# Performance work log

Measured on AMD Instinct MI355X. Metric: run time of the kernel, lower is better.

## Reference

```python
import jax, jax.numpy as jnp
import numpy as np

B, T, D, H, L, V = 2, 1024, 1024, 4, 4, 32000  # H redefined below
H = 16            # n_heads
HD = D // H       # head_size = 64
NL = 4            # n_layer
EPS = 1e-5


def _layernorm(x, scale, bias):
    mu = jnp.mean(x, axis=-1, keepdims=True)
    var = jnp.mean(jnp.square(x - mu), axis=-1, keepdims=True)
    return (x - mu) * jax.lax.rsqrt(var + EPS) * scale + bias


def setup_inputs() -> dict:
    key = jax.random.key(0)
    ks = iter(jax.random.split(key, 40))
    s = lambda shape: jax.random.normal(next(ks), shape, jnp.float32) * 0.02
    inp = {
        'idx': jax.random.randint(next(ks), (B, T), 0, V),
        'tok_emb': s((V, D)),
        'pos_emb': s((T, D)),
        # per-layer stacked params (leading axis = layer)
        'Wq': s((NL, D, D)), 'Wk': s((NL, D, D)), 'Wv': s((NL, D, D)),
        'Wo': s((NL, D, D)), 'bo': jnp.zeros((NL, D), jnp.float32),
        'ln1_s': jnp.ones((NL, D), jnp.float32), 'ln1_b': jnp.zeros((NL, D), jnp.float32),
        'ln2_s': jnp.ones((NL, D), jnp.float32), 'ln2_b': jnp.zeros((NL, D), jnp.float32),
        'W1': s((NL, D, 4 * D)), 'b1': jnp.zeros((NL, 4 * D), jnp.float32),
        'W2': s((NL, 4 * D, D)), 'b2': jnp.zeros((NL, D), jnp.float32),
        'lnf_s': jnp.ones((D,), jnp.float32), 'lnf_b': jnp.zeros((D,), jnp.float32),
        'Wlm': s((D, V)), 'blm': jnp.zeros((V,), jnp.float32),
    }
    return inp


def reference(idx, tok_emb, pos_emb, Wq, Wk, Wv, Wo, bo,
              ln1_s, ln1_b, ln2_s, ln2_b, W1, b1, W2, b2,
              lnf_s, lnf_b, Wlm, blm):
    b, t = idx.shape
    x = tok_emb[idx] + pos_emb[None, :t]            # [B,T,D]
    causal = jnp.tril(jnp.ones((t, t), bool))        # [T,T]
    scale = 1.0 / np.sqrt(HD).astype(np.float32)
    for l in range(NL):
        h = _layernorm(x, ln1_s[l], ln1_b[l])
        q = (h @ Wq[l]).reshape(b, t, H, HD)
        k = (h @ Wk[l]).reshape(b, t, H, HD)
        v = (h @ Wv[l]).reshape(b, t, H, HD)
        scores = jnp.einsum('bthd,bshd->bhts', q, k) * scale
        scores = jnp.where(causal[None, None], scores, -jnp.inf)
        attn = jax.nn.softmax(scores, axis=-1)       # [B,H,T,T]
        o = jnp.einsum('bhts,bshd->bthd', attn, v).reshape(b, t, D)
        x = x + o @ Wo[l] + bo[l]
        h2 = _layernorm(x, ln2_s[l], ln2_b[l])
        x = x + jax.nn.relu(h2 @ W1[l] + b1[l]) @ W2[l] + b2[l]
    x = _layernorm(x, lnf_s, lnf_b)
    logits = x @ Wlm + blm                           # [B,T,V]
    return logits
```

## Files before the change

### kernel.cpp

```cpp
#include <hip/hip_runtime.h>

typedef unsigned short u16;
typedef unsigned int u32;
typedef __bf16 bf16x8 __attribute__((ext_vector_type(8)));
typedef float f32x4 __attribute__((ext_vector_type(4)));
typedef u16 u16x8 __attribute__((ext_vector_type(8)));
typedef u16 u16x4 __attribute__((ext_vector_type(4)));

static __device__ __forceinline__ u16 f2bf(float f) {
  u32 u = __builtin_bit_cast(u32, f);
  u32 r = (u + 0x7FFFu + ((u >> 16) & 1u)) >> 16;
  return (u16)r;
}

static __device__ __forceinline__ void atomAddF32(float* p, float v) {
  asm volatile("global_atomic_add_f32 %0, %1, off" :: "v"(p), "v"(v) : "memory");
}

#define GLOAD_LDS16(gp, lp)                                                   \
  __builtin_amdgcn_global_load_lds(                                           \
      (const __attribute__((address_space(1))) void*)(gp),                    \
      (__attribute__((address_space(3))) void*)(lp), 16, 0, 0)

__global__ void k_embed_ln(const int* __restrict__ idx, const float* __restrict__ tok,
                           const float* __restrict__ pos, const float* __restrict__ sc,
                           const float* __restrict__ bi, float* __restrict__ x,
                           u16* __restrict__ out) {
  int row = blockIdx.x;
  int tt = row & 1023;
  int id = idx[row];
  int t = threadIdx.x;
  float4 a = *(const float4*)(tok + (size_t)id * 1024 + t * 4);
  float4 p = *(const float4*)(pos + (size_t)tt * 1024 + t * 4);
  float4 v{a.x + p.x, a.y + p.y, a.z + p.z, a.w + p.w};
  *(float4*)(x + (size_t)row * 1024 + t * 4) = v;
  float s = v.x + v.y + v.z + v.w;
  float ss = v.x * v.x + v.y * v.y + v.z * v.z + v.w * v.w;
  for (int d = 1; d < 64; d <<= 1) { s += __shfl_xor(s, d); ss += __shfl_xor(ss, d); }
  __shared__ float red[8];
  int wave = t >> 6, lane = t & 63;
  if (lane == 0) { red[wave] = s; red[wave + 4] = ss; }
  __syncthreads();
  s = red[0] + red[1] + red[2] + red[3];
  ss = red[4] + red[5] + red[6] + red[7];
  float mu = s * (1.0f / 1024.0f);
  float var = ss * (1.0f / 1024.0f) - mu * mu;
  float inv = rsqrtf(var + 1e-5f);
  float4 g = *(const float4*)(sc + t * 4);
  float4 b = *(const float4*)(bi + t * 4);
  u16x4 o;
  o[0] = f2bf((v.x - mu) * inv * g.x + b.x);
  o[1] = f2bf((v.y - mu) * inv * g.y + b.y);
  o[2] = f2bf((v.z - mu) * inv * g.z + b.z);
  o[3] = f2bf((v.w - mu) * inv * g.w + b.w);
  *(u16x4*)(out + (size_t)row * 1024 + t * 4) = o;
}

__global__ void k_ln(const float* __restrict__ x, const float* __restrict__ sc,
                     const float* __restrict__ bi, u16* __restrict__ out) {
  int row = blockIdx.x;
  int t = threadIdx.x;
  const float* xr = x + (size_t)row * 1024;
  float4 v = *(const float4*)(xr + t * 4);
  float s = v.x + v.y + v.z + v.w;
  float ss = v.x * v.x + v.y * v.y + v.z * v.z + v.w * v.w;
  for (int d = 1; d < 64; d <<= 1) { s += __shfl_xor(s, d); ss += __shfl_xor(ss, d); }
  __shared__ float red[8];
  int wave = t >> 6, lane = t & 63;
  if (lane == 0) { red[wave] = s; red[wave + 4] = ss; }
  __syncthreads();
  s = red[0] + red[1] + red[2] + red[3];
  ss = red[4] + red[5] + red[6] + red[7];
  float mu = s * (1.0f / 1024.0f);
  float var = ss * (1.0f / 1024.0f) - mu * mu;
  float inv = rsqrtf(var + 1e-5f);
  float4 g = *(const float4*)(sc + t * 4);
  float4 b = *(const float4*)(bi + t * 4);
  u16x4 o;
  o[0] = f2bf((v.x - mu) * inv * g.x + b.x);
  o[1] = f2bf((v.y - mu) * inv * g.y + b.y);
  o[2] = f2bf((v.z - mu) * inv * g.z + b.z);
  o[3] = f2bf((v.w - mu) * inv * g.w + b.w);
  *(u16x4*)(out + (size_t)row * 1024 + t * 4) = o;
}

__launch_bounds__(1024)
__global__ void k_transpose(const float* __restrict__ src, u16* __restrict__ dst,
                            int R, int C) {
  __shared__ float tile[32][33];
  int tx = threadIdx.x, ty = threadIdx.y;
  int c = blockIdx.x * 32 + tx;
  int r = blockIdx.y * 32 + ty;
  tile[ty][tx] = src[(size_t)r * C + c];
  __syncthreads();
  int dr = blockIdx.x * 32 + ty;
  int dc = blockIdx.y * 32 + tx;
  dst[(size_t)dr * R + dc] = f2bf(tile[tx][ty]);
}

__launch_bounds__(1024)
__global__ void k_transpose_layer(const float* __restrict__ Wq, const float* __restrict__ Wk,
                                  const float* __restrict__ Wv, const float* __restrict__ Wo,
                                  const float* __restrict__ W1, const float* __restrict__ W2,
                                  u16* __restrict__ qkvT, u16* __restrict__ WoT,
                                  u16* __restrict__ W1T, u16* __restrict__ W2T) {
  int bid = blockIdx.x;
  const float* src; u16* dst; int R, C, bx, by;
  if (bid < 4096) {
    int which = bid >> 10, tile_i = bid & 1023;
    bx = tile_i & 31; by = tile_i >> 5; R = 1024; C = 1024;
    src = which == 0 ? Wq : which == 1 ? Wk : which == 2 ? Wv : Wo;
    dst = which == 3 ? WoT : qkvT + (size_t)which * 1048576;
  } else if (bid < 8192) {
    int tile_i = bid - 4096; bx = tile_i & 127; by = tile_i >> 7; R = 1024; C = 4096;
    src = W1; dst = W1T;
  } else {
    int tile_i = bid - 8192; bx = tile_i & 31; by = tile_i >> 5; R = 4096; C = 1024;
    src = W2; dst = W2T;
  }
  __shared__ float tile[32][33];
  int tx = threadIdx.x, ty = threadIdx.y;
  int c = bx * 32 + tx, r = by * 32 + ty;
  tile[ty][tx] = src[(size_t)r * C + c];
  __syncthreads();
  int dr = bx * 32 + ty, dc = by * 32 + tx;
  dst[(size_t)dr * R + dc] = f2bf(tile[tx][ty]);
}

enum { EPI_QKV = 0, EPI_RELU = 2 };

template <int EPI>
__launch_bounds__(256, 4)
__global__ void k_gemm64(const u16* __restrict__ A, const u16* __restrict__ Bt,
                         const float* __restrict__ bias, u16* __restrict__ bout,
                         int M, int N, int K) {
  __shared__ alignas(16) u16 smem[12288];
#define AL(s, r, k) smem[(s)*2048 + (r)*32 + (k)]
#define BL(s, r, k) smem[4096 + (s)*4096 + (r)*32 + (k)]
  const int t = threadIdx.x;
  const int wave = t >> 6, lane = t & 63;
  const int wm = wave >> 1, wn = wave & 1;
  const int g = lane >> 4, c = lane & 15;
  const int m0 = blockIdx.x * 64, n0 = blockIdx.y * 128;

  const int rwA = t >> 2, sgA = (t & 3) * 8;
  const u16* gA = A + (size_t)(m0 + rwA) * K + sgA;
  const u16* gB = Bt + (size_t)(n0 + rwA) * K + sgA;

  f32x4 acc[2][4] = {};
  const int nK = K >> 5;
  int cur = 0;

  GLOAD_LDS16(gA, &AL(0, rwA, 0));
#pragma unroll
  for (int p = 0; p < 2; ++p)
    GLOAD_LDS16(gB + (size_t)p * 64 * K, &BL(0, p * 64 + rwA, 0));
  __syncthreads();

  for (int kt = 0; kt < nK; ++kt) {
    if (kt + 1 < nK) {
      const int k0 = (kt + 1) << 5;
      GLOAD_LDS16(gA + k0, &AL(cur ^ 1, rwA, 0));
#pragma unroll
      for (int p = 0; p < 2; ++p)
        GLOAD_LDS16(gB + k0 + (size_t)p * 64 * K, &BL(cur ^ 1, p * 64 + rwA, 0));
    }
    bf16x8 af[2], bfr[4];
#pragma unroll
    for (int i = 0; i < 2; ++i)
      af[i] = *(const bf16x8*)&AL(cur, wm * 32 + i * 16 + c, g * 8);
#pragma unroll
    for (int j = 0; j < 4; ++j)
      bfr[j] = *(const bf16x8*)&BL(cur, wn * 64 + j * 16 + c, g * 8);
#pragma unroll
    for (int i = 0; i < 2; ++i)
#pragma unroll
      for (int j = 0; j < 4; ++j)
        acc[i][j] = __builtin_amdgcn_mfma_f32_16x16x32_bf16(af[i], bfr[j], acc[i][j], 0, 0, 0);
    __syncthreads();
    cur ^= 1;
  }

  if (EPI == EPI_QKV) {
    const int which = n0 >> 10;
    const int b = m0 >> 10, t0 = m0 & 1023;
    const int hh0 = (n0 >> 6) & 15;
    if (which < 2) {
      u16 (*Ct)[136] = (u16(*)[136])smem;
#pragma unroll
      for (int i = 0; i < 2; ++i)
#pragma unroll
        for (int j = 0; j < 4; ++j)
#pragma unroll
          for (int r = 0; r < 4; ++r)
            Ct[wm * 32 + i * 16 + g * 4 + r][wn * 64 + j * 16 + c] = f2bf(acc[i][j][r]);
      __syncthreads();
      u16* obase = bout + (size_t)which * 2097152;
#pragma unroll
      for (int itr = 0; itr < 4; ++itr) {
        int idx2 = itr * 256 + t;
        int s = idx2 >> 9;
        int tt = (idx2 >> 3) & 63;
        int seg = idx2 & 7;
        u16x8 vv = *(const u16x8*)&Ct[tt][s * 64 + seg * 8];
        *(u16x8*)(obase + ((size_t)(b * 16 + hh0 + s) * 1024 + (t0 + tt)) * 64 + seg * 8) = vv;
      }
    } else {
      u16 (*Cv)[72] = (u16(*)[72])smem;
#pragma unroll
      for (int i = 0; i < 2; ++i)
#pragma unroll
        for (int j = 0; j < 4; ++j) {
          u16x4 pk;
#pragma unroll
          for (int r = 0; r < 4; ++r) pk[r] = f2bf(acc[i][j][r]);
          *(u16x4*)&Cv[wn * 64 + j * 16 + c][wm * 32 + i * 16 + g * 4] = pk;
        }
      __syncthreads();
      u16* obase = bout + (size_t)2 * 2097152;
#pragma unroll
      for (int itr = 0; itr < 4; ++itr) {
        int idx2 = itr * 256 + t;
        int row = idx2 >> 3;
        int seg = idx2 & 7;
        int s = row >> 6, f = row & 63;
        u16x8 vv = *(const u16x8*)&Cv[row][seg * 8];
        *(u16x8*)(obase + ((size_t)(b * 16 + hh0 + s) * 64 + f) * 1024 + t0 + seg * 8) = vv;
      }
    }
  } else {
    u16 (*Ct)[136] = (u16(*)[136])smem;
#pragma unroll
    for (int i = 0; i < 2; ++i)
#pragma unroll
      for (int j = 0; j < 4; ++j)
#pragma unroll
        for (int r = 0; r < 4; ++r) {
          float u = acc[i][j][r] + bias[n0 + wn * 64 + j * 16 + c];
          Ct[wm * 32 + i * 16 + g * 4 + r][wn * 64 + j * 16 + c] = f2bf(u > 0.f ? u : 0.f);
        }
    __syncthreads();
#pragma unroll
    for (int itr = 0; itr < 4; ++itr) {
      int idx2 = itr * 256 + t;
      int tt = idx2 >> 4, seg = idx2 & 15;
      *(u16x8*)(bout + (size_t)(m0 + tt) * N + n0 + seg * 8) =
          *(const u16x8*)&Ct[tt][seg * 8];
    }
  }
#undef AL
#undef BL
}

__launch_bounds__(256, 8)
__global__ void k_gemm_res(const u16* __restrict__ A, const u16* __restrict__ Bt,
                           const float* __restrict__ bias, float* __restrict__ fout,
                           int M, int N, int K) {
  __shared__ alignas(16) u16 smem[8192];
  const int t = threadIdx.x;
  const int wave = t >> 6, lane = t & 63;
  const int wm = wave >> 1, wn = wave & 1;
  const int g = lane >> 4, c = lane & 15;
  const int m0 = blockIdx.x * 64, n0 = blockIdx.y * 64;
  const int kz = blockIdx.z;
  const int Kh = K >> 1;
  const int kbase = kz * Kh;

  const int rw = t >> 2, sg = (t & 3) * 8;
  const u16* gA = A + (size_t)(m0 + rw) * K + kbase + sg;
  const u16* gB = Bt + (size_t)(n0 + rw) * K + kbase + sg;

  f32x4 acc[2][2] = {};
  const int nK = Kh >> 5;
  int cur = 0;

  GLOAD_LDS16(gA, &smem[rw * 32]);
  GLOAD_LDS16(gB, &smem[4096 + rw * 32]);
  __syncthreads();

  for (int kt = 0; kt < nK; ++kt) {
    if (kt + 1 < nK) {
      const int k0 = (kt + 1) << 5;
      GLOAD_LDS16(gA + k0, &smem[(cur ^ 1) * 2048 + rw * 32]);
      GLOAD_LDS16(gB + k0, &smem[4096 + (cur ^ 1) * 2048 + rw * 32]);
    }
    bf16x8 af[2], bfr[2];
#pragma unroll
    for (int i = 0; i < 2; ++i)
      af[i] = *(const bf16x8*)&smem[cur * 2048 + (wm * 32 + i * 16 + c) * 32 + g * 8];
#pragma unroll
    for (int j = 0; j < 2; ++j)
      bfr[j] = *(const bf16x8*)&smem[4096 + cur * 2048 + (wn * 32 + j * 16 + c) * 32 + g * 8];
#pragma unroll
    for (int i = 0; i < 2; ++i)
#pragma unroll
      for (int j = 0; j < 2; ++j)
        acc[i][j] = __builtin_amdgcn_mfma_f32_16x16x32_bf16(af[i], bfr[j], acc[i][j], 0, 0, 0);
    __syncthreads();
    cur ^= 1;
  }

#pragma unroll
  for (int i = 0; i < 2; ++i)
#pragma unroll
    for (int j = 0; j < 2; ++j)
#pragma unroll
      for (int r = 0; r < 4; ++r) {
        int m = m0 + wm * 32 + i * 16 + g * 4 + r;
        int n = n0 + wn * 32 + j * 16 + c;
        float v = acc[i][j][r] + (kz == 0 ? bias[n] : 0.f);
        atomAddF32(&fout[(size_t)m * N + n], v);
      }
}

__launch_bounds__(256, 4)
__global__ void k_gemm_out(const u16* __restrict__ A, const u16* __restrict__ Bt,
                           const float* __restrict__ bias, float* __restrict__ fout,
                           int M, int N, int K) {
  __shared__ alignas(16) u16 sm[2][2][128][32];
  const int t = threadIdx.x;
  const int wave = t >> 6, lane = t & 63;
  const int wm = wave >> 1, wn = wave & 1;
  const int g = lane >> 4, c = lane & 15;
  const int wg = (blockIdx.x & 7) * 500 + (blockIdx.x >> 3);
  const int m0 = (wg & 15) * 128, n0 = (wg >> 4) * 128;

  const int srow = wave * 32 + (lane >> 2);
  const int sseg = (lane & 3) * 8;
  const u16* gA = A + (size_t)(m0 + srow) * K + sseg;
  const u16* gB = Bt + (size_t)(n0 + srow) * K + sseg;

  f32x4 acc[4][4] = {};
  const int nK = K >> 5;
  int cur = 0;

#pragma unroll
  for (int p = 0; p < 2; ++p) {
    GLOAD_LDS16(gA + (size_t)p * 16 * K, &sm[0][0][wave * 32 + p * 16][0]);
    GLOAD_LDS16(gB + (size_t)p * 16 * K, &sm[0][1][wave * 32 + p * 16][0]);
  }
  __syncthreads();

  for (int kt = 0; kt < nK; ++kt) {
    if (kt + 1 < nK) {
      const int k0 = (kt + 1) << 5;
#pragma unroll
      for (int p = 0; p < 2; ++p) {
        GLOAD_LDS16(gA + k0 + (size_t)p * 16 * K, &sm[cur ^ 1][0][wave * 32 + p * 16][0]);
        GLOAD_LDS16(gB + k0 + (size_t)p * 16 * K, &sm[cur ^ 1][1][wave * 32 + p * 16][0]);
      }
    }
    bf16x8 af[4], bfr[4];
#pragma unroll
    for (int i = 0; i < 4; ++i) {
      af[i]  = *(const bf16x8*)&sm[cur][0][wm * 64 + i * 16 + c][g * 8];
      bfr[i] = *(const bf16x8*)&sm[cur][1][wn * 64 + i * 16 + c][g * 8];
    }
#pragma unroll
    for (int i = 0; i < 4; ++i)
#pragma unroll
      for (int j = 0; j < 4; ++j)
        acc[i][j] = __builtin_amdgcn_mfma_f32_16x16x32_bf16(af[i], bfr[j], acc[i][j], 0, 0, 0);
    __syncthreads();
    cur ^= 1;
  }

  float (*st)[132] = (float(*)[132])sm;
#pragma unroll
  for (int i = 0; i < 4; ++i) {
#pragma unroll
    for (int j = 0; j < 4; ++j)
#pragma unroll
      for (int r = 0; r < 4; ++r)
        st[wm * 16 + g * 4 + r][wn * 64 + j * 16 + c] = acc[i][j][r];
    __syncthreads();
    {
      int row = t >> 3;
      int cs = (t & 7) * 16;
      int m = m0 + (row >> 4) * 64 + i * 16 + (row & 15);
      float* dst = fout + (size_t)m * N + n0 + cs;
#pragma unroll
      for (int q = 0; q < 4; ++q) {
        float4 v = *(const float4*)&st[row][cs + q * 4];
        float4 bb = *(const float4*)&bias[n0 + cs + q * 4];
        float4 o{v.x + bb.x, v.y + bb.y, v.z + bb.z, v.w + bb.w};
        *(float4*)(dst + q * 4) = o;
      }
    }
    __syncthreads();
  }
}

__launch_bounds__(128)
__global__ void k_attn(const u16* __restrict__ Q, const u16* __restrict__ Kb,
                       const u16* __restrict__ VT, u16* __restrict__ O) {
  const int qb = blockIdx.x;
  const int bh = blockIdx.y;
  const int tid = threadIdx.x;
  const int wv = tid >> 6;
  const int lane = tid & 63;
  const int g = lane >> 4, c = lane & 15;
  const int q0 = qb << 5;
  const u16* Qh = Q + (size_t)bh * 65536;
  const u16* Kh = Kb + (size_t)bh * 65536;
  const u16* VTh = VT + (size_t)bh * 65536;

  __shared__ u16 Pl[2][32][40];
  __shared__ float mrg[64][48];

  bf16x8 aq[2][2];
#pragma unroll
  for (int qt = 0; qt < 2; ++qt) {
    aq[qt][0] = *(const bf16x8*)(Qh + (q0 + qt * 16 + c) * 64 + g * 8);
    aq[qt][1] = *(const bf16x8*)(Qh + (q0 + qt * 16 + c) * 64 + 32 + g * 8);
  }

  f32x4 Oacc[2][4] = {};
  float Mr[2][4], Lr[2][4] = {};
#pragma unroll
  for (int qt = 0; qt < 2; ++qt)
#pragma unroll
    for (int r = 0; r < 4; ++r) Mr[qt][r] = -1e30f;

  const int nIt = qb + 1;
  const int half = (nIt + 1) >> 1;
  const int itBeg = wv ? half : 0;
  const int itEnd = wv ? nIt : half;

  for (int it = itBeg; it < itEnd; ++it) {
    const int k0 = it << 5;
    bf16x8 b0 = *(const bf16x8*)(Kh + (k0 + c) * 64 + g * 8);
    bf16x8 b1 = *(const bf16x8*)(Kh + (k0 + c) * 64 + 32 + g * 8);
    bf16x8 b2 = *(const bf16x8*)(Kh + (k0 + 16 + c) * 64 + g * 8);
    bf16x8 b3 = *(const bf16x8*)(Kh + (k0 + 16 + c) * 64 + 32 + g * 8);
    f32x4 S[2][2];
#pragma unroll
    for (int qt = 0; qt < 2; ++qt) {
      f32x4 z = {};
      S[qt][0] = __builtin_amdgcn_mfma_f32_16x16x32_bf16(
          aq[qt][1], b1, __builtin_amdgcn_mfma_f32_16x16x32_bf16(aq[qt][0], b0, z, 0, 0, 0), 0, 0, 0);
      S[qt][1] = __builtin_amdgcn_mfma_f32_16x16x32_bf16(
          aq[qt][1], b3, __builtin_amdgcn_mfma_f32_16x16x32_bf16(aq[qt][0], b2, z, 0, 0, 0), 0, 0, 0);
    }
    const float scale = 0.125f;
    float sv[2][2][4], mt[2][4];
    float need = 0.0f;
#pragma unroll
    for (int qt = 0; qt < 2; ++qt)
#pragma unroll
      for (int r = 0; r < 4; ++r) {
        int q = q0 + qt * 16 + (g << 2) + r;
        float s0 = (k0 + c <= q) ? S[qt][0][r] * scale : -1e30f;
        float s1 = (k0 + 16 + c <= q) ? S[qt][1][r] * scale : -1e30f;
        sv[qt][0][r] = s0; sv[qt][1][r] = s1;
        float m = fmaxf(s0, s1);
        m = fmaxf(m, __shfl_xor(m, 1));
        m = fmaxf(m, __shfl_xor(m, 2));
        m = fmaxf(m, __shfl_xor(m, 4));
        m = fmaxf(m, __shfl_xor(m, 8));
        mt[qt][r] = m;
        need = fmaxf(need, m - Mr[qt][r]);
      }
    unsigned long long vote = __ballot(need <= 8.0f);
    const bool nore = wv ? ((vote >> 32) == 0xFFFFFFFFull ? true : ((vote & 0xFFFFFFFF00000000ull) == 0xFFFFFFFF00000000ull))
                         : ((vote & 0xFFFFFFFFull) == 0xFFFFFFFFull);
#pragma unroll
    for (int qt = 0; qt < 2; ++qt)
#pragma unroll
      for (int r = 0; r < 4; ++r) {
        float mn = nore ? Mr[qt][r] : fmaxf(Mr[qt][r], mt[qt][r]);
        float p0 = __expf(sv[qt][0][r] - mn);
        float p1 = __expf(sv[qt][1][r] - mn);
        float rs = p0 + p1;
        rs += __shfl_xor(rs, 1);
        rs += __shfl_xor(rs, 2);
        rs += __shfl_xor(rs, 4);
        rs += __shfl_xor(rs, 8);
        if (nore) {
          Lr[qt][r] += rs;
        } else {
          float alpha = __expf(Mr[qt][r] - mn);
          Lr[qt][r] = Lr[qt][r] * alpha + rs;
          Mr[qt][r] = mn;
#pragma unroll
          for (int nb = 0; nb < 4; ++nb) Oacc[qt][nb][r] *= alpha;
        }
        Pl[wv][qt * 16 + (g << 2) + r][c] = f2bf(p0);
        Pl[wv][qt * 16 + (g << 2) + r][16 + c] = f2bf(p1);
      }
#pragma unroll
    for (int nb = 0; nb < 4; ++nb) {
      bf16x8 bv = *(const bf16x8*)(VTh + (size_t)(nb * 16 + c) * 1024 + k0 + g * 8);
#pragma unroll
      for (int qt = 0; qt < 2; ++qt) {
        bf16x8 ap = *(const bf16x8*)&Pl[wv][qt * 16 + c][g * 8];
        Oacc[qt][nb] = __builtin_amdgcn_mfma_f32_16x16x32_bf16(ap, bv, Oacc[qt][nb], 0, 0, 0);
      }
    }
  }

  if (wv == 1) {
#pragma unroll
    for (int qt = 0; qt < 2; ++qt) {
#pragma unroll
      for (int nb = 0; nb < 4; ++nb)
#pragma unroll
        for (int r = 0; r < 4; ++r)
          mrg[lane][qt * 16 + nb * 4 + r] = Oacc[qt][nb][r];
#pragma unroll
      for (int r = 0; r < 4; ++r) {
        mrg[lane][32 + qt * 4 + r] = Mr[qt][r];
        mrg[lane][40 + qt * 4 + r] = Lr[qt][r];
      }
    }
  }
  __syncthreads();
  if (wv == 0) {
    const int b = bh >> 4, hh = bh & 15;
#pragma unroll
    for (int qt = 0; qt < 2; ++qt)
#pragma unroll
      for (int r = 0; r < 4; ++r) {
        float m1 = mrg[lane][32 + qt * 4 + r];
        float l1 = mrg[lane][40 + qt * 4 + r];
        float mm = fmaxf(Mr[qt][r], m1);
        float a0 = __expf(Mr[qt][r] - mm);
        float a1 = __expf(m1 - mm);
        float l = a0 * Lr[qt][r] + a1 * l1;
        float invl = 1.0f / l;
        int tt = q0 + qt * 16 + (g << 2) + r;
#pragma unroll
        for (int nb = 0; nb < 4; ++nb) {
          float o1 = mrg[lane][qt * 16 + nb * 4 + r];
          float val = (a0 * Oacc[qt][nb][r] + a1 * o1) * invl;
          int d = nb * 16 + c;
          O[((size_t)(b * 1024 + tt)) * 1024 + hh * 64 + d] = f2bf(val);
        }
      }
  }
}

extern "C" void kernel_launch(void* const* d_in, const int* in_sizes, int n_in,
                              void* d_out, int out_size, void* d_ws, size_t ws_size,
                              hipStream_t stream) {
  const int*   idx  = (const int*)d_in[0];
  const float* tok  = (const float*)d_in[1];
  const float* pos  = (const float*)d_in[2];
  const float* Wq   = (const float*)d_in[3];
  const float* Wk   = (const float*)d_in[4];
  const float* Wv   = (const float*)d_in[5];
  const float* Wo   = (const float*)d_in[6];
  const float* bo   = (const float*)d_in[7];
  const float* ln1s = (const float*)d_in[8];
  const float* ln1b = (const float*)d_in[9];
  const float* ln2s = (const float*)d_in[10];
  const float* ln2b = (const float*)d_in[11];
  const float* W1   = (const float*)d_in[12];
  const float* b1   = (const float*)d_in[13];
  const float* W2   = (const float*)d_in[14];
  const float* b2   = (const float*)d_in[15];
  const float* lnfs = (const float*)d_in[16];
  const float* lnfb = (const float*)d_in[17];
  const float* Wlm  = (const float*)d_in[18];
  const float* blm  = (const float*)d_in[19];
  float* out = (float*)d_out;

  char* w = (char*)d_ws;
  auto alloc = [&](size_t bytes) {
    char* p = w;
    w += (bytes + 255) & ~(size_t)255;
    return p;
  };
  float* x  = (float*)alloc(2048ull * 1024 * 4);
  u16* h    = (u16*)alloc(2048ull * 1024 * 2);
  u16* qkv  = (u16*)alloc(3ull * 2097152 * 2);
  u16* o    = (u16*)alloc(2048ull * 1024 * 2);
  u16* a1   = (u16*)alloc(2048ull * 4096 * 2);
  u16* arena = (u16*)alloc(32000ull * 1024 * 2);

  dim3 b32(32, 32, 1);

  k_embed_ln<<<2048, 256, 0, stream>>>(idx, tok, pos, ln1s, ln1b, x, h);

  for (int l = 0; l < 4; ++l) {
    u16* qkvT = arena;
    u16* WoT  = arena + 3ull * 1048576;
    u16* W1T  = arena + 4ull * 1048576;
    u16* W2T  = arena + 8ull * 1048576;
    k_transpose_layer<<<12288, b32, 0, stream>>>(
        Wq + (size_t)l * 1048576, Wk + (size_t)l * 1048576,
        Wv + (size_t)l * 1048576, Wo + (size_t)l * 1048576,
        W1 + (size_t)l * 4194304, W2 + (size_t)l * 4194304,
        qkvT, WoT, W1T, W2T);

    if (l > 0)
      k_ln<<<2048, 256, 0, stream>>>(x, ln1s + l * 1024, ln1b + l * 1024, h);
    k_gemm64<EPI_QKV><<<dim3(32, 24), 256, 0, stream>>>(h, qkvT, nullptr, qkv,
                                                        2048, 3072, 1024);
    k_attn<<<dim3(32, 32), 128, 0, stream>>>(qkv, qkv + 2097152, qkv + 2 * 2097152, o);
    k_gemm_res<<<dim3(32, 16, 2), 256, 0, stream>>>(o, WoT, bo + l * 1024, x,
                                                    2048, 1024, 1024);
    k_ln<<<2048, 256, 0, stream>>>(x, ln2s + l * 1024, ln2b + l * 1024, h);
    k_gemm64<EPI_RELU><<<dim3(32, 32), 256, 0, stream>>>(h, W1T, b1 + l * 4096, a1,
                                                         2048, 4096, 1024);
    k_gemm_res<<<dim3(32, 16, 2), 256, 0, stream>>>(a1, W2T, b2 + l * 1024, x,
                                                    2048, 1024, 4096);
  }

  k_ln<<<2048, 256, 0, stream>>>(x, lnfs, lnfb, h);
  k_transpose<<<dim3(1000, 32), b32, 0, stream>>>(Wlm, arena, 1024, 32000);
  k_gemm_out<<<4000, 256, 0, stream>>>(h, arena, blm, out, 2048, 32000, 1024);
}
```

Measured before the change: 1.137 ms.

## Triple-buffer GEMM LDS stages with partial vmcnt waits

Converts the three GEMM kernels from double-buffered to triple-buffered LDS staging, prefetching two K-tiles ahead. Each iteration now waits with a partial s_waitcnt vmcnt plus a barrier instead of a full __syncthreads, so the next tile's loads stay in flight while the current one is consumed. This raises LDS use per block, which may lower occupancy. It also simplifies a redundant ballot expression in attention.

Result: no change. 1.150 ms (+1.1%).

```diff
diff --git a/kernel.cpp b/kernel.cpp
--- a/kernel.cpp
+++ b/kernel.cpp
@@ -21,6 +21,9 @@
   __builtin_amdgcn_global_load_lds(                                           \
       (const __attribute__((address_space(1))) void*)(gp),                    \
       (__attribute__((address_space(3))) void*)(lp), 16, 0, 0)
+
+#define WBAR(Ns)                                                              \
+  asm volatile("s_waitcnt vmcnt(" Ns ")\ns_waitcnt lgkmcnt(0)\ns_barrier" ::: "memory")
 
 __global__ void k_embed_ln(const int* __restrict__ idx, const float* __restrict__ tok,
                            const float* __restrict__ pos, const float* __restrict__ sc,
@@ -134,9 +137,16 @@
 __global__ void k_gemm64(const u16* __restrict__ A, const u16* __restrict__ Bt,
                          const float* __restrict__ bias, u16* __restrict__ bout,
                          int M, int N, int K) {
-  __shared__ alignas(16) u16 smem[12288];
-#define AL(s, r, k) smem[(s)*2048 + (r)*32 + (k)]
-#define BL(s, r, k) smem[4096 + (s)*4096 + (r)*32 + (k)]
+  __shared__ alignas(16) u16 smem[18432];
+#define AL(s, r, k) smem[(s)*6144 + (r)*32 + (k)]
+#define BL(s, r, k) smem[(s)*6144 + 2048 + (r)*32 + (k)]
+#define STG64(buf, kt)                                                        \
+  {                                                                           \
+    const int k0s = (kt) << 5;                                                \
+    GLOAD_LDS16(gA + k0s, &AL(buf, rwA, 0));                                  \
+    _Pragma("unroll") for (int p = 0; p < 2; ++p)                             \
+      GLOAD_LDS16(gB + k0s + (size_t)p * 64 * K, &BL(buf, p * 64 + rwA, 0));  \
+  }
   const int t = threadIdx.x;
   const int wave = t >> 6, lane = t & 63;
   const int wm = wave >> 1, wn = wave & 1;
@@ -151,20 +161,13 @@
   const int nK = K >> 5;
   int cur = 0;
 
-  GLOAD_LDS16(gA, &AL(0, rwA, 0));
-#pragma unroll
-  for (int p = 0; p < 2; ++p)
-    GLOAD_LDS16(gB + (size_t)p * 64 * K, &BL(0, p * 64 + rwA, 0));
-  __syncthreads();
+  STG64(0, 0); STG64(1, 1);
+  WBAR("3");
 
   for (int kt = 0; kt < nK; ++kt) {
-    if (kt + 1 < nK) {
-      const int k0 = (kt + 1) << 5;
-      GLOAD_LDS16(gA + k0, &AL(cur ^ 1, rwA, 0));
-#pragma unroll
-      for (int p = 0; p < 2; ++p)
-        GLOAD_LDS16(gB + k0 + (size_t)p * 64 * K, &BL(cur ^ 1, p * 64 + rwA, 0));
-    }
+    const int sb = cur == 0 ? 2 : cur - 1;
+    const bool more2 = (kt + 2 < nK);
+    if (more2) STG64(sb, kt + 2);
     bf16x8 af[2], bfr[4];
 #pragma unroll
     for (int i = 0; i < 2; ++i)
@@ -177,9 +180,12 @@
 #pragma unroll
       for (int j = 0; j < 4; ++j)
         acc[i][j] = __builtin_amdgcn_mfma_f32_16x16x32_bf16(af[i], bfr[j], acc[i][j], 0, 0, 0);
-    __syncthreads();
-    cur ^= 1;
-  }
+    if (kt + 1 < nK) {
+      if (more2) WBAR("3"); else WBAR("0");
+    }
+    cur = (cur == 2) ? 0 : cur + 1;
+  }
+  __syncthreads();
 
   if (EPI == EPI_QKV) {
     const int which = n0 >> 10;
@@ -250,13 +256,22 @@
   }
 #undef AL
 #undef BL
+#undef STG64
 }
 
 __launch_bounds__(256, 8)
 __global__ void k_gemm_res(const u16* __restrict__ A, const u16* __restrict__ Bt,
                            const float* __restrict__ bias, float* __restrict__ fout,
                            int M, int N, int K) {
-  __shared__ alignas(16) u16 smem[8192];
+  __shared__ alignas(16) u16 smem[12288];
+#define ALr(s, r, k) smem[(s)*4096 + (r)*32 + (k)]
+#define BLr(s, r, k) smem[(s)*4096 + 2048 + (r)*32 + (k)]
+#define STGR(buf, kt)                                                         \
+  {                                                                           \
+    const int k0s = (kt) << 5;                                                \
+    GLOAD_LDS16(gA + k0s, &ALr(buf, rw, 0));                                  \
+    GLOAD_LDS16(gB + k0s, &BLr(buf, rw, 0));                                  \
+  }
   const int t = threadIdx.x;
   const int wave = t >> 6, lane = t & 63;
   const int wm = wave >> 1, wn = wave & 1;
@@ -274,30 +289,29 @@
   const int nK = Kh >> 5;
   int cur = 0;
 
-  GLOAD_LDS16(gA, &smem[rw * 32]);
-  GLOAD_LDS16(gB, &smem[4096 + rw * 32]);
-  __syncthreads();
+  STGR(0, 0); STGR(1, 1);
+  WBAR("2");
 
   for (int kt = 0; kt < nK; ++kt) {
-    if (kt + 1 < nK) {
-      const int k0 = (kt + 1) << 5;
-      GLOAD_LDS16(gA + k0, &smem[(cur ^ 1) * 2048 + rw * 32]);
-      GLOAD_LDS16(gB + k0, &smem[4096 + (cur ^ 1) * 2048 + rw * 32]);
-    }
+    const int sb = cur == 0 ? 2 : cur - 1;
+    const bool more2 = (kt + 2 < nK);
+    if (more2) STGR(sb, kt + 2);
     bf16x8 af[2], bfr[2];
 #pragma unroll
     for (int i = 0; i < 2; ++i)
-      af[i] = *(const bf16x8*)&smem[cur * 2048 + (wm * 32 + i * 16 + c) * 32 + g * 8];
+      af[i] = *(const bf16x8*)&ALr(cur, wm * 32 + i * 16 + c, g * 8);
 #pragma unroll
     for (int j = 0; j < 2; ++j)
-      bfr[j] = *(const bf16x8*)&smem[4096 + cur * 2048 + (wn * 32 + j * 16 + c) * 32 + g * 8];
+      bfr[j] = *(const bf16x8*)&BLr(cur, wn * 32 + j * 16 + c, g * 8);
 #pragma unroll
     for (int i = 0; i < 2; ++i)
 #pragma unroll
       for (int j = 0; j < 2; ++j)
         acc[i][j] = __builtin_amdgcn_mfma_f32_16x16x32_bf16(af[i], bfr[j], acc[i][j], 0, 0, 0);
-    __syncthreads();
-    cur ^= 1;
+    if (kt + 1 < nK) {
+      if (more2) WBAR("2"); else WBAR("0");
+    }
+    cur = (cur == 2) ? 0 : cur + 1;
   }
 
 #pragma unroll
@@ -311,13 +325,24 @@
         float v = acc[i][j][r] + (kz == 0 ? bias[n] : 0.f);
         atomAddF32(&fout[(size_t)m * N + n], v);
       }
+#undef ALr
+#undef BLr
+#undef STGR
 }
 
 __launch_bounds__(256, 4)
 __global__ void k_gemm_out(const u16* __restrict__ A, const u16* __restrict__ Bt,
                            const float* __restrict__ bias, float* __restrict__ fout,
                            int M, int N, int K) {
-  __shared__ alignas(16) u16 sm[2][2][128][32];
+  __shared__ alignas(16) u16 sm[3][2][128][32];
+#define STGO(buf, kt)                                                         \
+  {                                                                           \
+    const int k0s = (kt) << 5;                                                \
+    _Pragma("unroll") for (int p = 0; p < 2; ++p) {                           \
+      GLOAD_LDS16(gA + k0s + (size_t)p * 16 * K, &sm[buf][0][wave * 32 + p * 16][0]); \
+      GLOAD_LDS16(gB + k0s + (size_t)p * 16 * K, &sm[buf][1][wave * 32 + p * 16][0]); \
+    }                                                                         \
+  }
   const int t = threadIdx.x;
   const int wave = t >> 6, lane = t & 63;
   const int wm = wave >> 1, wn = wave & 1;
@@ -334,22 +359,13 @@
   const int nK = K >> 5;
   int cur = 0;
 
-#pragma unroll
-  for (int p = 0; p < 2; ++p) {
-    GLOAD_LDS16(gA + (size_t)p * 16 * K, &sm[0][0][wave * 32 + p * 16][0]);
-    GLOAD_LDS16(gB + (size_t)p * 16 * K, &sm[0][1][wave * 32 + p * 16][0]);
-  }
-  __syncthreads();
+  STGO(0, 0); STGO(1, 1);
+  WBAR("4");
 
   for (int kt = 0; kt < nK; ++kt) {
-    if (kt + 1 < nK) {
-      const int k0 = (kt + 1) << 5;
-#pragma unroll
-      for (int p = 0; p < 2; ++p) {
-        GLOAD_LDS16(gA + k0 + (size_t)p * 16 * K, &sm[cur ^ 1][0][wave * 32 + p * 16][0]);
-        GLOAD_LDS16(gB + k0 + (size_t)p * 16 * K, &sm[cur ^ 1][1][wave * 32 + p * 16][0]);
-      }
-    }
+    const int sb = cur == 0 ? 2 : cur - 1;
+    const bool more2 = (kt + 2 < nK);
+    if (more2) STGO(sb, kt + 2);
     bf16x8 af[4], bfr[4];
 #pragma unroll
     for (int i = 0; i < 4; ++i) {
@@ -361,9 +377,12 @@
 #pragma unroll
       for (int j = 0; j < 4; ++j)
         acc[i][j] = __builtin_amdgcn_mfma_f32_16x16x32_bf16(af[i], bfr[j], acc[i][j], 0, 0, 0);
-    __syncthreads();
-    cur ^= 1;
-  }
+    if (kt + 1 < nK) {
+      if (more2) WBAR("4"); else WBAR("0");
+    }
+    cur = (cur == 2) ? 0 : cur + 1;
+  }
+  __syncthreads();
 
   float (*st)[132] = (float(*)[132])sm;
 #pragma unroll
@@ -389,6 +408,7 @@
     }
     __syncthreads();
   }
+#undef STGO
 }
 
 __launch_bounds__(128)
@@ -462,7 +482,7 @@
         need = fmaxf(need, m - Mr[qt][r]);
       }
     unsigned long long vote = __ballot(need <= 8.0f);
-    const bool nore = wv ? ((vote >> 32) == 0xFFFFFFFFull ? true : ((vote & 0xFFFFFFFF00000000ull) == 0xFFFFFFFF00000000ull))
+    const bool nore = wv ? ((vote & 0xFFFFFFFF00000000ull) == 0xFFFFFFFF00000000ull)
                          : ((vote & 0xFFFFFFFFull) == 0xFFFFFFFFull);
 #pragma unroll
     for (int qt = 0; qt < 2; ++qt)
```

## Specialize attention loop for unmasked tiles and defer row-sum reduction

Applied to the files above, without the earlier changes.

The attention inner loop becomes a macro that is instantiated separately for masked (diagonal) and unmasked tiles, so causal masking runs only on the last block. The softmax scale is folded into the Q projection epilogue, and the per-iteration cross-lane row-sum shuffles are replaced by a single reduction at the merge step. V loads are hoisted before the QK MFMAs, and s_setprio is raised around the MFMA sections. This cuts ALU and shuffle work per iteration. In exchange it adds code size and relies on the wave split so that the diagonal tile always lands on the expected wave.

Result: faster. 1.070 ms (-5.9%).

```diff
diff --git a/kernel.cpp b/kernel.cpp
--- a/kernel.cpp
+++ b/kernel.cpp
@@ -21,6 +21,8 @@
   __builtin_amdgcn_global_load_lds(                                           \
       (const __attribute__((address_space(1))) void*)(gp),                    \
       (__attribute__((address_space(3))) void*)(lp), 16, 0, 0)
+
+#define MFB(a, b, cc) __builtin_amdgcn_mfma_f32_16x16x32_bf16(a, b, cc, 0, 0, 0)
 
 __global__ void k_embed_ln(const int* __restrict__ idx, const float* __restrict__ tok,
                            const float* __restrict__ pos, const float* __restrict__ sc,
@@ -176,7 +178,7 @@
     for (int i = 0; i < 2; ++i)
 #pragma unroll
       for (int j = 0; j < 4; ++j)
-        acc[i][j] = __builtin_amdgcn_mfma_f32_16x16x32_bf16(af[i], bfr[j], acc[i][j], 0, 0, 0);
+        acc[i][j] = MFB(af[i], bfr[j], acc[i][j]);
     __syncthreads();
     cur ^= 1;
   }
@@ -186,6 +188,7 @@
     const int b = m0 >> 10, t0 = m0 & 1023;
     const int hh0 = (n0 >> 6) & 15;
     if (which < 2) {
+      const float qsc = (which == 0) ? 0.125f : 1.0f;
       u16 (*Ct)[136] = (u16(*)[136])smem;
 #pragma unroll
       for (int i = 0; i < 2; ++i)
@@ -193,7 +196,7 @@
         for (int j = 0; j < 4; ++j)
 #pragma unroll
           for (int r = 0; r < 4; ++r)
-            Ct[wm * 32 + i * 16 + g * 4 + r][wn * 64 + j * 16 + c] = f2bf(acc[i][j][r]);
+            Ct[wm * 32 + i * 16 + g * 4 + r][wn * 64 + j * 16 + c] = f2bf(acc[i][j][r] * qsc);
       __syncthreads();
       u16* obase = bout + (size_t)which * 2097152;
 #pragma unroll
@@ -295,7 +298,7 @@
     for (int i = 0; i < 2; ++i)
 #pragma unroll
       for (int j = 0; j < 2; ++j)
-        acc[i][j] = __builtin_amdgcn_mfma_f32_16x16x32_bf16(af[i], bfr[j], acc[i][j], 0, 0, 0);
+        acc[i][j] = MFB(af[i], bfr[j], acc[i][j]);
     __syncthreads();
     cur ^= 1;
   }
@@ -360,7 +363,7 @@
     for (int i = 0; i < 4; ++i)
 #pragma unroll
       for (int j = 0; j < 4; ++j)
-        acc[i][j] = __builtin_amdgcn_mfma_f32_16x16x32_bf16(af[i], bfr[j], acc[i][j], 0, 0, 0);
+        acc[i][j] = MFB(af[i], bfr[j], acc[i][j]);
     __syncthreads();
     cur ^= 1;
   }
@@ -390,6 +393,74 @@
     __syncthreads();
   }
 }
+
+#define AITER(ITV, MASKED)                                                    \
+  {                                                                           \
+    const int k0 = (ITV) << 5;                                                \
+    bf16x8 kb0 = *(const bf16x8*)(Kh + (k0 + c) * 64 + g * 8);                \
+    bf16x8 kb1 = *(const bf16x8*)(Kh + (k0 + c) * 64 + 32 + g * 8);           \
+    bf16x8 kb2 = *(const bf16x8*)(Kh + (k0 + 16 + c) * 64 + g * 8);           \
+    bf16x8 kb3 = *(const bf16x8*)(Kh + (k0 + 16 + c) * 64 + 32 + g * 8);      \
+    bf16x8 bv0 = *(const bf16x8*)(VTh + (size_t)(c) * 1024 + k0 + g * 8);     \
+    bf16x8 bv1 = *(const bf16x8*)(VTh + (size_t)(16 + c) * 1024 + k0 + g * 8);\
+    bf16x8 bv2 = *(const bf16x8*)(VTh + (size_t)(32 + c) * 1024 + k0 + g * 8);\
+    bf16x8 bv3 = *(const bf16x8*)(VTh + (size_t)(48 + c) * 1024 + k0 + g * 8);\
+    f32x4 S[2][2];                                                            \
+    __builtin_amdgcn_s_setprio(1);                                            \
+    _Pragma("unroll") for (int qt = 0; qt < 2; ++qt) {                        \
+      f32x4 z = {};                                                           \
+      S[qt][0] = MFB(aq[qt][1], kb1, MFB(aq[qt][0], kb0, z));                 \
+      S[qt][1] = MFB(aq[qt][1], kb3, MFB(aq[qt][0], kb2, z));                 \
+    }                                                                         \
+    __builtin_amdgcn_s_setprio(0);                                            \
+    float sv[2][2][4], mt[2][4];                                              \
+    float need = 0.0f;                                                        \
+    _Pragma("unroll") for (int qt = 0; qt < 2; ++qt)                          \
+      _Pragma("unroll") for (int r = 0; r < 4; ++r) {                         \
+        float s0 = S[qt][0][r], s1 = S[qt][1][r];                             \
+        if (MASKED) {                                                         \
+          int q = q0 + qt * 16 + (g << 2) + r;                                \
+          s0 = (k0 + c <= q) ? s0 : -1e30f;                                   \
+          s1 = (k0 + 16 + c <= q) ? s1 : -1e30f;                              \
+        }                                                                     \
+        sv[qt][0][r] = s0; sv[qt][1][r] = s1;                                 \
+        float m = fmaxf(s0, s1);                                              \
+        m = fmaxf(m, __shfl_xor(m, 1));                                       \
+        m = fmaxf(m, __shfl_xor(m, 2));                                       \
+        m = fmaxf(m, __shfl_xor(m, 4));                                       \
+        m = fmaxf(m, __shfl_xor(m, 8));                                       \
+        mt[qt][r] = m;                                                        \
+        need = fmaxf(need, m - Mr[qt][r]);                                    \
+      }                                                                       \
+    unsigned long long vote = __ballot(need <= 8.0f);                         \
+    const bool nore = wv ? ((vote & 0xFFFFFFFF00000000ull) == 0xFFFFFFFF00000000ull) \
+                         : ((vote & 0xFFFFFFFFull) == 0xFFFFFFFFull);         \
+    _Pragma("unroll") for (int qt = 0; qt < 2; ++qt)                          \
+      _Pragma("unroll") for (int r = 0; r < 4; ++r) {                         \
+        float mn = nore ? Mr[qt][r] : fmaxf(Mr[qt][r], mt[qt][r]);            \
+        float p0 = __expf(sv[qt][0][r] - mn);                                 \
+        float p1 = __expf(sv[qt][1][r] - mn);                                 \
+        if (nore) {                                                           \
+          Lr[qt][r] += p0 + p1;         \
+        } else {                                                              \
+          float alpha = __expf(Mr[qt][r] - mn);                               \
+          Lr[qt][r] = Lr[qt][r] * alpha + p0 + p1;                            \
+          Mr[qt][r] = mn;                                                     \
+          _Pragma("unroll") for (int nb = 0; nb < 4; ++nb) Oacc[qt][nb][r] *= alpha; \
+        }                                                                     \
+        Pl[wv][qt * 16 + (g << 2) + r][c] = f2bf(p0);                         \
+        Pl[wv][qt * 16 + (g << 2) + r][16 + c] = f2bf(p1);                    \
+      }                                                                       \
+    __builtin_amdgcn_s_setprio(1);                                            \
+    _Pragma("unroll") for (int qt = 0; qt < 2; ++qt) {                        \
+      bf16x8 ap = *(const bf16x8*)&Pl[wv][qt * 16 + c][g * 8];                \
+      Oacc[qt][0] = MFB(ap, bv0, Oacc[qt][0]);                                \
+      Oacc[qt][1] = MFB(ap, bv1, Oacc[qt][1]);                                \
+      Oacc[qt][2] = MFB(ap, bv2, Oacc[qt][2]);                                \
+      Oacc[qt][3] = MFB(ap, bv3, Oacc[qt][3]);                                \
+    }                                                                         \
+    __builtin_amdgcn_s_setprio(0);                                            \
+  }
 
 __launch_bounds__(128)
 __global__ void k_attn(const u16* __restrict__ Q, const u16* __restrict__ Kb,
@@ -424,79 +495,16 @@
 
   const int nIt = qb + 1;
   const int half = (nIt + 1) >> 1;
-  const int itBeg = wv ? half : 0;
-  const int itEnd = wv ? nIt : half;
-
-  for (int it = itBeg; it < itEnd; ++it) {
-    const int k0 = it << 5;
-    bf16x8 b0 = *(const bf16x8*)(Kh + (k0 + c) * 64 + g * 8);
-    bf16x8 b1 = *(const bf16x8*)(Kh + (k0 + c) * 64 + 32 + g * 8);
-    bf16x8 b2 = *(const bf16x8*)(Kh + (k0 + 16 + c) * 64 + g * 8);
-    bf16x8 b3 = *(const bf16x8*)(Kh + (k0 + 16 + c) * 64 + 32 + g * 8);
-    f32x4 S[2][2];
-#pragma unroll
-    for (int qt = 0; qt < 2; ++qt) {
-      f32x4 z = {};
-      S[qt][0] = __builtin_amdgcn_mfma_f32_16x16x32_bf16(
-          aq[qt][1], b1, __builtin_amdgcn_mfma_f32_16x16x32_bf16(aq[qt][0], b0, z, 0, 0, 0), 0, 0, 0);
-      S[qt][1] = __builtin_amdgcn_mfma_f32_16x16x32_bf16(
-          aq[qt][1], b3, __builtin_amdgcn_mfma_f32_16x16x32_bf16(aq[qt][0], b2, z, 0, 0, 0), 0, 0, 0);
-    }
-    const float scale = 0.125f;
-    float sv[2][2][4], mt[2][4];
-    float need = 0.0f;
-#pragma unroll
-    for (int qt = 0; qt < 2; ++qt)
-#pragma unroll
-      for (int r = 0; r < 4; ++r) {
-        int q = q0 + qt * 16 + (g << 2) + r;
-        float s0 = (k0 + c <= q) ? S[qt][0][r] * scale : -1e30f;
-        float s1 = (k0 + 16 + c <= q) ? S[qt][1][r] * scale : -1e30f;
-        sv[qt][0][r] = s0; sv[qt][1][r] = s1;
-        float m = fmaxf(s0, s1);
-        m = fmaxf(m, __shfl_xor(m, 1));
-        m = fmaxf(m, __shfl_xor(m, 2));
-        m = fmaxf(m, __shfl_xor(m, 4));
-        m = fmaxf(m, __shfl_xor(m, 8));
-        mt[qt][r] = m;
-        need = fmaxf(need, m - Mr[qt][r]);
-      }
-    unsigned long long vote = __ballot(need <= 8.0f);
-    const bool nore = wv ? ((vote >> 32) == 0xFFFFFFFFull ? true : ((vote & 0xFFFFFFFF00000000ull) == 0xFFFFFFFF00000000ull))
-                         : ((vote & 0xFFFFFFFFull) == 0xFFFFFFFFull);
-#pragma unroll
-    for (int qt = 0; qt < 2; ++qt)
-#pragma unroll
-      for (int r = 0; r < 4; ++r) {
-        float mn = nore ? Mr[qt][r] : fmaxf(Mr[qt][r], mt[qt][r]);
-        float p0 = __expf(sv[qt][0][r] - mn);
-        float p1 = __expf(sv[qt][1][r] - mn);
-        float rs = p0 + p1;
-        rs += __shfl_xor(rs, 1);
-        rs += __shfl_xor(rs, 2);
-        rs += __shfl_xor(rs, 4);
-        rs += __shfl_xor(rs, 8);
-        if (nore) {
-          Lr[qt][r] += rs;
-        } else {
-          float alpha = __expf(Mr[qt][r] - mn);
-          Lr[qt][r] = Lr[qt][r] * alpha + rs;
-          Mr[qt][r] = mn;
-#pragma unroll
-          for (int nb = 0; nb < 4; ++nb) Oacc[qt][nb][r] *= alpha;
-        }
-        Pl[wv][qt * 16 + (g << 2) + r][c] = f2bf(p0);
-        Pl[wv][qt * 16 + (g << 2) + r][16 + c] = f2bf(p1);
-      }
-#pragma unroll
-    for (int nb = 0; nb < 4; ++nb) {
-      bf16x8 bv = *(const bf16x8*)(VTh + (size_t)(nb * 16 + c) * 1024 + k0 + g * 8);
-#pragma unroll
-      for (int qt = 0; qt < 2; ++qt) {
-        bf16x8 ap = *(const bf16x8*)&Pl[wv][qt * 16 + c][g * 8];
-        Oacc[qt][nb] = __builtin_amdgcn_mfma_f32_16x16x32_bf16(ap, bv, Oacc[qt][nb], 0, 0, 0);
-      }
-    }
+
+  if (wv == 0) {
+    if (qb == 0) {
+      AITER(0, 1);
+    } else {
+      for (int it = 0; it < half; ++it) AITER(it, 0);
+    }
+  } else {
+    for (int it = half; it < nIt - 1; ++it) AITER(it, 0);
+    if (qb >= 1) AITER(nIt - 1, 1);
   }
 
   if (wv == 1) {
@@ -527,6 +535,10 @@
         float a0 = __expf(Mr[qt][r] - mm);
         float a1 = __expf(m1 - mm);
         float l = a0 * Lr[qt][r] + a1 * l1;
+        l += __shfl_xor(l, 1);
+        l += __shfl_xor(l, 2);
+        l += __shfl_xor(l, 4);
+        l += __shfl_xor(l, 8);
         float invl = 1.0f / l;
         int tt = q0 + qt * 16 + (g << 2) + r;
 #pragma unroll
```
